# Performance work log

Measured on AMD Instinct MI355X. Metric: run time of the kernel, lower is better.

Reference implementation:

```python
import jax, jax.numpy as jnp
import numpy as np

N_NODES = 100000
N_EDGES = 1600000
D_IN = 128
D_OUT = 128


def setup_inputs() -> dict:
    key = jax.random.key(0)
    k1, k2, k3, k4, k5 = jax.random.split(key, 5)
    features = jax.random.normal(k1, (N_NODES, D_IN), dtype=jnp.float32)
    edge_row = jax.random.randint(k2, (N_EDGES,), 0, N_NODES, dtype=jnp.int32)
    edge_col = jax.random.randint(k3, (N_EDGES,), 0, N_NODES, dtype=jnp.int32)
    edge_val = jax.random.uniform(k4, (N_EDGES,), dtype=jnp.float32)
    # Xavier-uniform weight, zero bias, ones skip weight (matches reset_parameters)
    limit = float(np.sqrt(6.0 / (D_IN + D_OUT)))
    weight = jax.random.uniform(k5, (D_IN, D_OUT), minval=-limit, maxval=limit, dtype=jnp.float32)
    bias = jnp.zeros((D_OUT,), dtype=jnp.float32)
    skip_weight = jnp.ones((D_OUT,), dtype=jnp.float32)
    return {"features": features, "edge_row": edge_row, "edge_col": edge_col,
            "edge_val": edge_val, "weight": weight, "bias": bias,
            "skip_weight": skip_weight}


def reference(features, edge_row, edge_col, edge_val, weight, bias, skip_weight):
    # Dense projection: [N, Din] @ [Din, Dout] -> [N, Dout]
    h = features @ weight
    # SpMM in COO form: Ah[r] = sum_e val[e] * h[col[e]] for edges with row[e]==r
    gathered = edge_val[:, None] * h[edge_col]          # [E, Dout]
    Ah = jax.ops.segment_sum(gathered, edge_row, num_segments=N_NODES)
    # Skip-scale + bias + activation epilogue
    out = h * skip_weight[None, :] + Ah + bias[None, :]
    return jax.nn.selu(out)
```

## Files before the change

### kernel.cpp

```cpp
#include <hip/hip_runtime.h>

#define N_NODES 100000
#define N_EDGES 1600000
#define D 128
#define BM 64
#define GEMM_BLKS 1563

#define BROWS 128
#define NB 782
#define EB 250
#define EPB 6400
#define NTAB (NB * EB)
#define SCAN_BLKS 191

#define SPMM_BLKS 6250

typedef __attribute__((ext_vector_type(8))) short short8_t;
typedef __attribute__((ext_vector_type(4))) float float4_t;
typedef __attribute__((ext_vector_type(2))) float f32x2_t;

__device__ __forceinline__ unsigned pack_bf16x2(float a, float b) {
    unsigned ua = __float_as_uint(a);
    unsigned ub = __float_as_uint(b);
    ua = (ua + 0x7fffu + ((ua >> 16) & 1u)) >> 16;
    ub = (ub + 0x7fffu + ((ub >> 16) & 1u)) & 0xffff0000u;
    return ua | ub;
}

__device__ __forceinline__ float selu_f(float x) {
    const float SCALE = 1.0507009873554805f;
    const float ALPHA = 1.6732632423543772f;
    return x > 0.f ? SCALE * x : SCALE * ALPHA * (expf(x) - 1.f);
}

__global__ __launch_bounds__(256) void bhist_prep_kernel(
    const int* __restrict__ erow, const float* __restrict__ W,
    unsigned* __restrict__ tbl, unsigned short* __restrict__ wt)
{
    __shared__ unsigned hcnt[NB];
    const int t = threadIdx.x;
    if (blockIdx.x < EB) {
        const int k = blockIdx.x;
        for (int i = t; i < NB; i += 256) hcnt[i] = 0;
        __syncthreads();
        const int4* q = (const int4*)(erow + k * EPB);
        for (int i = t; i < EPB / 4; i += 256) {
            const int4 r = q[i];
            atomicAdd(&hcnt[r.x >> 7], 1u);
            atomicAdd(&hcnt[r.y >> 7], 1u);
            atomicAdd(&hcnt[r.z >> 7], 1u);
            atomicAdd(&hcnt[r.w >> 7], 1u);
        }
        __syncthreads();
        for (int i = t; i < NB; i += 256) tbl[k * NB + i] = hcnt[i];
    } else {
        const int pb = blockIdx.x - EB;
        for (int idx = pb * 4096 + t; idx < (pb + 1) * 4096; idx += 256) {
            const int k = idx >> 7, n = idx & 127;
            unsigned u = __float_as_uint(W[idx]);
            u = (u + 0x7fffu + ((u >> 16) & 1u)) >> 16;
            wt[n * D + k] = (unsigned short)u;
        }
    }
}

__global__ __launch_bounds__(1024) void scan_local_kernel(
    const unsigned* __restrict__ tbl, unsigned* __restrict__ lex,
    unsigned* __restrict__ bsum)
{
    __shared__ unsigned wsum[16];
    const int t = threadIdx.x;
    const int L = blockIdx.x * 1024 + t;
    const int lane = t & 63;

    unsigned v = 0;
    if (L < NTAB) {
        const int b = L / EB;
        const int k = L - b * EB;
        v = tbl[k * NB + b];
    }
    unsigned x = v;
#pragma unroll
    for (int d = 1; d < 64; d <<= 1) {
        const unsigned y = __shfl_up(x, d, 64);
        if (lane >= d) x += y;
    }
    if (lane == 63) wsum[t >> 6] = x;
    __syncthreads();
    unsigned add = 0;
    for (int w = 0; w < (t >> 6); ++w) add += wsum[w];
    x += add;
    if (L < NTAB) lex[L] = x - v;
    if (t == 1023) bsum[blockIdx.x] = x;
}

__global__ __launch_bounds__(1024) void scan_apply_kernel(
    const unsigned* __restrict__ lex, const unsigned* __restrict__ bsum,
    unsigned* __restrict__ tbl)
{
    __shared__ unsigned ssum[16];
    __shared__ unsigned offs;
    const int t = threadIdx.x;

    unsigned v = (t < SCAN_BLKS && t < (int)blockIdx.x) ? bsum[t] : 0u;
#pragma unroll
    for (int d = 32; d >= 1; d >>= 1) v += __shfl_down(v, d, 64);
    if ((t & 63) == 0) ssum[t >> 6] = v;
    __syncthreads();
    if (t == 0) {
        unsigned s = 0;
#pragma unroll
        for (int i = 0; i < 16; ++i) s += ssum[i];
        offs = s;
    }
    __syncthreads();

    const int L = blockIdx.x * 1024 + t;
    if (L >= NTAB) return;
    const int b = L / EB;
    const int k = L - b * EB;
    tbl[k * NB + b] = lex[L] + offs;
}

__global__ __launch_bounds__(256) void gemm_scatter_kernel(
    const float* __restrict__ feat, const unsigned short* __restrict__ wt,
    unsigned* __restrict__ h16,
    const int* __restrict__ erow, const int* __restrict__ ecol,
    const float* __restrict__ eval_, const unsigned* __restrict__ tbl,
    int2* __restrict__ rec)
{
    __shared__ __align__(16) char smem[52224];
    const int t = threadIdx.x;

    if (blockIdx.x < GEMM_BLKS) {
        short* At = (short*)smem;
        short* Wt = (short*)(smem + 17408);
        const int rowBase = blockIdx.x * BM;

        {
            const int n = t >> 1, hf = t & 1;
            const uint4* src = (const uint4*)(wt + n * D + hf * 64);
            uint4* dst = (uint4*)&Wt[n * 136 + hf * 64];
#pragma unroll
            for (int j = 0; j < 8; ++j) dst[j] = src[j];
        }
        {
#pragma unroll
            for (int i = 0; i < 8; ++i) {
                const int p = t + 256 * i;
                const int r = p >> 5, kq = p & 31;
                int row = rowBase + r;
                if (row >= N_NODES) row = N_NODES - 1;
                const float4 f = *(const float4*)&feat[(size_t)row * D + kq * 4];
                uint2 u;
                u.x = pack_bf16x2(f.x, f.y);
                u.y = pack_bf16x2(f.z, f.w);
                *(uint2*)&At[r * 136 + kq * 4] = u;
            }
        }
        __syncthreads();

        const int w = t >> 6, lane = t & 63;
        const int m16 = lane & 15, kg = lane >> 4;

        short8_t a_frag[4];
        const int arow = w * 16 + m16;
#pragma unroll
        for (int k0 = 0; k0 < 4; ++k0)
            a_frag[k0] = *(const short8_t*)&At[arow * 136 + k0 * 32 + kg * 8];

#pragma unroll
        for (int nt = 0; nt < 8; ++nt) {
            float4_t acc = {0.f, 0.f, 0.f, 0.f};
#pragma unroll
            for (int k0 = 0; k0 < 4; ++k0) {
                const short8_t b =
                    *(const short8_t*)&Wt[(nt * 16 + m16) * 136 + k0 * 32 + kg * 8];
                acc = __builtin_amdgcn_mfma_f32_16x16x32_bf16(a_frag[k0], b, acc, 0, 0, 0);
            }
            float mine[4], part[4];
#pragma unroll
            for (int i = 0; i < 4; ++i) {
                mine[i] = acc[i];
                part[i] = __shfl_xor(mine[i], 1, 64);
            }
            if ((m16 & 1) == 0) {
                const int cp = (nt * 16 + m16) >> 1;
#pragma unroll
                for (int i = 0; i < 4; ++i) {
                    const int row = rowBase + w * 16 + kg * 4 + i;
                    if (row < N_NODES)
                        h16[(size_t)row * 64 + cp] = pack_bf16x2(mine[i], part[i]);
                }
            }
        }
    } else {
        unsigned* rk = (unsigned*)smem;
        const int k = blockIdx.x - GEMM_BLKS;
        for (int i = t; i < NB; i += 256) rk[i] = 0;
        __syncthreads();

        const int4*   qr = (const int4*)(erow + k * EPB);
        const int4*   qc = (const int4*)(ecol + k * EPB);
        const float4* qv = (const float4*)(eval_ + k * EPB);
        const unsigned* base = tbl + k * NB;

        for (int i = t; i < EPB / 4; i += 256) {
            const int4   r = qr[i];
            const int4   c = qc[i];
            const float4 v = qv[i];
            {
                const int b = r.x >> 7;
                const unsigned pos = base[b] + atomicAdd(&rk[b], 1u);
                rec[pos] = make_int2(c.x | ((r.x & 127) << 17), __float_as_int(v.x));
            }
            {
                const int b = r.y >> 7;
                const unsigned pos = base[b] + atomicAdd(&rk[b], 1u);
                rec[pos] = make_int2(c.y | ((r.y & 127) << 17), __float_as_int(v.y));
            }
            {
                const int b = r.z >> 7;
                const unsigned pos = base[b] + atomicAdd(&rk[b], 1u);
                rec[pos] = make_int2(c.z | ((r.z & 127) << 17), __float_as_int(v.z));
            }
            {
                const int b = r.w >> 7;
                const unsigned pos = base[b] + atomicAdd(&rk[b], 1u);
                rec[pos] = make_int2(c.w | ((r.w & 127) << 17), __float_as_int(v.w));
            }
        }
    }
}

__global__ __launch_bounds__(256) void bsort_kernel(
    const unsigned* __restrict__ tbl, const int2* __restrict__ rec,
    int2* __restrict__ rec2, unsigned* __restrict__ rstart)
{
    __shared__ unsigned cnt[BROWS], base[BROWS], rk[BROWS];
    __shared__ unsigned w0tot;
    const int t = threadIdx.x, b = blockIdx.x;
    if (t < BROWS) { cnt[t] = 0; rk[t] = 0; }
    __syncthreads();

    const unsigned s = tbl[b];
    const unsigned e = (b == NB - 1) ? N_EDGES : tbl[b + 1];

    for (unsigned j = s + t; j < e; j += 256)
        atomicAdd(&cnt[(rec[j].x >> 17) & 127], 1u);
    __syncthreads();

    unsigned v = 0, x = 0;
    if (t < BROWS) {
        v = cnt[t]; x = v;
#pragma unroll
        for (int d = 1; d < 64; d <<= 1) {
            const unsigned y = __shfl_up(x, d, 64);
            if ((t & 63) >= d) x += y;
        }
    }
    if (t == 63) w0tot = x;
    __syncthreads();
    if (t < BROWS) {
        const unsigned ex = x - v + ((t >= 64) ? w0tot : 0u);
        base[t] = s + ex;
        const int row = b * BROWS + t;
        if (row < N_NODES) rstart[row] = s + ex;
    }
    __syncthreads();

    for (unsigned j = s + t; j < e; j += 256) {
        const int2 R = rec[j];
        const int rl = (R.x >> 17) & 127;
        const unsigned pos = base[rl] + atomicAdd(&rk[rl], 1u);
        rec2[pos] = R;
    }
}

__global__ __launch_bounds__(256) void spmm_csr_kernel(
    const unsigned* __restrict__ rstart, const int2* __restrict__ rec,
    const unsigned* __restrict__ h16, const float* __restrict__ skip,
    const float* __restrict__ bias, float* __restrict__ out)
{
    const int lane = threadIdx.x & 63;
    const int wid  = threadIdx.x >> 6;
    const int rowBase = (blockIdx.x * 4 + wid) * 4;

    const int c2 = lane * 2;
    const float2 sk = *(const float2*)&skip[c2];
    const float2 bs = *(const float2*)&bias[c2];

    unsigned sb[5];
#pragma unroll
    for (int i = 0; i < 5; ++i) {
        const int rr = rowBase + i;
        const unsigned bnd = (rr < N_NODES) ? rstart[rr] : (unsigned)N_EDGES;
        sb[i] = (unsigned)__builtin_amdgcn_readfirstlane((int)bnd);
    }

#pragma unroll
    for (int r = 0; r < 4; ++r) {
        const int row = rowBase + r;
        const unsigned s = sb[r];
        const unsigned e = sb[r + 1];
        const unsigned n = e - s;
        const unsigned nfull = n >> 3;

        float ax = 0.f, ay = 0.f, bx = 0.f, by = 0.f;

        int2 E0[8], E1[8];
        unsigned g0[8], g1[8];

        auto LOADREC = [&](int2 (&E)[8], unsigned base) {
#pragma unroll
            for (int k = 0; k < 8; ++k) E[k] = rec[base + k];
        };
        auto GATHER = [&](unsigned (&g)[8], const int2 (&E)[8]) {
#pragma unroll
            for (int k = 0; k < 8; ++k)
                g[k] = h16[(size_t)(((unsigned)E[k].x) & 0x1FFFFu) * 64 + lane];
        };
        auto FMA8 = [&](const int2 (&E)[8], const unsigned (&g)[8]) {
#pragma unroll
            for (int k = 0; k < 8; ++k) {
                const float v = __int_as_float(E[k].y);
                if (k & 1) {
                    bx = fmaf(v, __uint_as_float(g[k] << 16), bx);
                    by = fmaf(v, __uint_as_float(g[k] & 0xffff0000u), by);
                } else {
                    ax = fmaf(v, __uint_as_float(g[k] << 16), ax);
                    ay = fmaf(v, __uint_as_float(g[k] & 0xffff0000u), ay);
                }
            }
        };

        if (nfull) {
            LOADREC(E0, s);
            GATHER(g0, E0);
            unsigned bi = 1;
            for (; bi + 1 < nfull; bi += 2) {
                LOADREC(E1, s + bi * 8);
                GATHER(g1, E1);
                FMA8(E0, g0);
                LOADREC(E0, s + (bi + 1) * 8);
                GATHER(g0, E0);
                FMA8(E1, g1);
            }
            if (bi < nfull) {
                LOADREC(E1, s + bi * 8);
                GATHER(g1, E1);
                FMA8(E0, g0);
                FMA8(E1, g1);
            } else {
                FMA8(E0, g0);
            }
        }

        const unsigned tn = n & 7;
        if (tn) {
            const unsigned tb = s + nfull * 8;
            int2 Et[8];
            unsigned gt[8];
#pragma unroll
            for (int k = 0; k < 8; ++k) {
                const unsigned idx = tb + (unsigned)k;
                Et[k] = rec[idx < e ? idx : e - 1u];
            }
#pragma unroll
            for (int k = 0; k < 8; ++k)
                gt[k] = h16[(size_t)(((unsigned)Et[k].x) & 0x1FFFFu) * 64 + lane];
#pragma unroll
            for (int k = 0; k < 8; ++k) {
                const float v = (tb + (unsigned)k < e) ? __int_as_float(Et[k].y) : 0.f;
                if (k & 1) {
                    bx = fmaf(v, __uint_as_float(gt[k] << 16), bx);
                    by = fmaf(v, __uint_as_float(gt[k] & 0xffff0000u), by);
                } else {
                    ax = fmaf(v, __uint_as_float(gt[k] << 16), ax);
                    ay = fmaf(v, __uint_as_float(gt[k] & 0xffff0000u), ay);
                }
            }
        }

        const unsigned hw = h16[(size_t)row * 64 + lane];
        float ox = fmaf(__uint_as_float(hw << 16),         sk.x, (ax + bx) + bs.x);
        float oy = fmaf(__uint_as_float(hw & 0xffff0000u), sk.y, (ay + by) + bs.y);
        ox = selu_f(ox);
        oy = selu_f(oy);
        f32x2_t o;
        o.x = ox;
        o.y = oy;
        __builtin_nontemporal_store(o, (f32x2_t*)&out[(size_t)row * D + c2]);
    }
}

__global__ __launch_bounds__(256) void gemm_fb_kernel(
    const float* __restrict__ feat, const float* __restrict__ W,
    const float* __restrict__ bias, const float* __restrict__ skip,
    float* __restrict__ h, float* __restrict__ out)
{
    __shared__ float Wl[D * D];
    __shared__ float Fl[32 * D];
    const int tid = threadIdx.x;

    const float4* W4 = (const float4*)W;
    float4* Wl4 = (float4*)Wl;
#pragma unroll
    for (int i = 0; i < 16; ++i) Wl4[tid + 256 * i] = W4[tid + 256 * i];

    const size_t rowBase = (size_t)blockIdx.x * 32;
    const float4* F4 = (const float4*)(feat + rowBase * D);
    float4* Fl4 = (float4*)Fl;
#pragma unroll
    for (int i = 0; i < 4; ++i) Fl4[tid + 256 * i] = F4[tid + 256 * i];
    __syncthreads();

    const int colg = (tid & 31) * 4;
    const int row0 = (tid >> 5) * 4;
    float4 acc[4];
#pragma unroll
    for (int r = 0; r < 4; ++r) acc[r] = make_float4(0.f, 0.f, 0.f, 0.f);
#pragma unroll 4
    for (int k = 0; k < D; ++k) {
        const float4 w = *(const float4*)&Wl[k * D + colg];
#pragma unroll
        for (int r = 0; r < 4; ++r) {
            const float aa = Fl[(row0 + r) * D + k];
            acc[r].x += aa * w.x; acc[r].y += aa * w.y;
            acc[r].z += aa * w.z; acc[r].w += aa * w.w;
        }
    }
    const float4 sk = *(const float4*)&skip[colg];
    const float4 bs = *(const float4*)&bias[colg];
#pragma unroll
    for (int r = 0; r < 4; ++r) {
        const size_t row = rowBase + row0 + r;
        *(float4*)&h[row * D + colg] = acc[r];
        float4 o;
        o.x = acc[r].x * sk.x + bs.x; o.y = acc[r].y * sk.y + bs.y;
        o.z = acc[r].z * sk.z + bs.z; o.w = acc[r].w * sk.w + bs.w;
        *(float4*)&out[row * D + colg] = o;
    }
}

__global__ __launch_bounds__(256) void spmm_atomic_kernel(
    const int* __restrict__ erow, const int* __restrict__ ecol,
    const float* __restrict__ eval_, const float* __restrict__ h,
    float* __restrict__ out)
{
    const int e = blockIdx.x * 4 + (threadIdx.x >> 6);
    if (e >= N_EDGES) return;
    const int lane = threadIdx.x & 63;
    const int r = erow[e];
    const int c = ecol[e];
    const float v = eval_[e];
    const float2 hv = *(const float2*)&h[(size_t)c * D + lane * 2];
    float* o = &out[(size_t)r * D + lane * 2];
    atomicAdd(o + 0, v * hv.x);
    atomicAdd(o + 1, v * hv.y);
}

__global__ __launch_bounds__(256) void selu_kernel(float* __restrict__ out)
{
    const size_t i = (size_t)blockIdx.x * blockDim.x + threadIdx.x;
    float4 v = ((float4*)out)[i];
    v.x = selu_f(v.x); v.y = selu_f(v.y); v.z = selu_f(v.z); v.w = selu_f(v.w);
    ((float4*)out)[i] = v;
}

extern "C" void kernel_launch(void* const* d_in, const int* in_sizes, int n_in,
                              void* d_out, int out_size, void* d_ws, size_t ws_size,
                              hipStream_t stream)
{
    const float* feat  = (const float*)d_in[0];
    const int*   erow  = (const int*)d_in[1];
    const int*   ecol  = (const int*)d_in[2];
    const float* eval_ = (const float*)d_in[3];
    const float* W     = (const float*)d_in[4];
    const float* bias  = (const float*)d_in[5];
    const float* skip  = (const float*)d_in[6];

    float* out = (float*)d_out;

    const size_t off_h16  = 0;
    const size_t off_tbl  = 25600000;
    const size_t off_lex  = 26382000;
    const size_t off_bs   = 27164336;
    const size_t off_rst  = 27165360;
    const size_t off_wt   = 27565360;
    const size_t off_rec  = 27598128;
    const size_t off_rec2 = 40398128;
    const size_t needed   = 53198128;

    char* ws = (char*)d_ws;
    unsigned*       h16    = (unsigned*)(ws + off_h16);
    unsigned*       tbl    = (unsigned*)(ws + off_tbl);
    unsigned*       lex    = (unsigned*)(ws + off_lex);
    unsigned*       bsum   = (unsigned*)(ws + off_bs);
    unsigned*       rstart = (unsigned*)(ws + off_rst);
    unsigned short* wt     = (unsigned short*)(ws + off_wt);
    int2*           rec    = (int2*)(ws + off_rec);
    int2*           rec2   = (int2*)(ws + off_rec2);

    if (ws_size >= needed) {
        bhist_prep_kernel<<<EB + 4, 256, 0, stream>>>(erow, W, tbl, wt);
        scan_local_kernel<<<SCAN_BLKS, 1024, 0, stream>>>(tbl, lex, bsum);
        scan_apply_kernel<<<SCAN_BLKS, 1024, 0, stream>>>(lex, bsum, tbl);
        gemm_scatter_kernel<<<GEMM_BLKS + EB, 256, 0, stream>>>(
            feat, wt, h16, erow, ecol, eval_, tbl, rec);
        bsort_kernel<<<NB, 256, 0, stream>>>(tbl, rec, rec2, rstart);
        spmm_csr_kernel<<<SPMM_BLKS, 256, 0, stream>>>(
            rstart, rec2, h16, skip, bias, out);
    } else {
        float* h = (float*)d_ws;
        gemm_fb_kernel<<<N_NODES / 32, 256, 0, stream>>>(feat, W, bias, skip, h, out);
        spmm_atomic_kernel<<<N_EDGES / 4, 256, 0, stream>>>(erow, ecol, eval_, h, out);
        selu_kernel<<<(N_NODES * D) / (256 * 4), 256, 0, stream>>>(out);
    }
}
```

Baseline: 134.7 us.

## Interleave SpMM gathers across four rows per wavefront to raise memory parallelism

Replaces the per-row software-pipelined gather loop with a joint loop that processes up to eight edges from each of the four rows a wave owns in every iteration. All record loads and gathers for the four rows are issued before the FMAs, so up to 32 gathers are in flight at once instead of 8–16 from a single row. Each chunk is masked with a tail predicate, which drops the separate full and tail paths. In exchange it uses more registers (4x8 records and gathers live at once), which may lower occupancy, and it loses the double-buffered prefetch across iterations.

```diff
diff --git a/kernel.cpp b/kernel.cpp
--- a/kernel.cpp
+++ b/kernel.cpp
@@ -298,93 +298,70 @@
         sb[i] = (unsigned)__builtin_amdgcn_readfirstlane((int)bnd);
     }
 
+    unsigned cur[4], end_[4];
+    float ax[4], ay[4], bx[4], by[4];
+#pragma unroll
+    for (int r = 0; r < 4; ++r) {
+        cur[r] = sb[r];
+        end_[r] = sb[r + 1];
+        ax[r] = 0.f; ay[r] = 0.f; bx[r] = 0.f; by[r] = 0.f;
+    }
+
+    bool more = (cur[0] < end_[0]) | (cur[1] < end_[1]) |
+                (cur[2] < end_[2]) | (cur[3] < end_[3]);
+    while (more) {
+        int2 Ebuf[4][8];
+        unsigned gbuf[4][8];
+        bool act[4];
+
+#pragma unroll
+        for (int r = 0; r < 4; ++r) {
+            act[r] = cur[r] < end_[r];
+            if (act[r]) {
+#pragma unroll
+                for (int k = 0; k < 8; ++k) {
+                    const unsigned idx = cur[r] + (unsigned)k;
+                    Ebuf[r][k] = rec[idx < end_[r] ? idx : end_[r] - 1u];
+                }
+            }
+        }
+#pragma unroll
+        for (int r = 0; r < 4; ++r) {
+            if (act[r]) {
+#pragma unroll
+                for (int k = 0; k < 8; ++k)
+                    gbuf[r][k] =
+                        h16[(size_t)(((unsigned)Ebuf[r][k].x) & 0x1FFFFu) * 64 + lane];
+            }
+        }
+        more = false;
+#pragma unroll
+        for (int r = 0; r < 4; ++r) {
+            if (act[r]) {
+#pragma unroll
+                for (int k = 0; k < 8; ++k) {
+                    const float v = (cur[r] + (unsigned)k < end_[r])
+                                        ? __int_as_float(Ebuf[r][k].y) : 0.f;
+                    if (k & 1) {
+                        bx[r] = fmaf(v, __uint_as_float(gbuf[r][k] << 16), bx[r]);
+                        by[r] = fmaf(v, __uint_as_float(gbuf[r][k] & 0xffff0000u), by[r]);
+                    } else {
+                        ax[r] = fmaf(v, __uint_as_float(gbuf[r][k] << 16), ax[r]);
+                        ay[r] = fmaf(v, __uint_as_float(gbuf[r][k] & 0xffff0000u), ay[r]);
+                    }
+                }
+                cur[r] += 8;
+            }
+            more = more || (cur[r] < end_[r]);
+        }
+    }
+
 #pragma unroll
     for (int r = 0; r < 4; ++r) {
         const int row = rowBase + r;
-        const unsigned s = sb[r];
-        const unsigned e = sb[r + 1];
-        const unsigned n = e - s;
-        const unsigned nfull = n >> 3;
-
-        float ax = 0.f, ay = 0.f, bx = 0.f, by = 0.f;
-
-        int2 E0[8], E1[8];
-        unsigned g0[8], g1[8];
-
-        auto LOADREC = [&](int2 (&E)[8], unsigned base) {
-#pragma unroll
-            for (int k = 0; k < 8; ++k) E[k] = rec[base + k];
-        };
-        auto GATHER = [&](unsigned (&g)[8], const int2 (&E)[8]) {
-#pragma unroll
-            for (int k = 0; k < 8; ++k)
-                g[k] = h16[(size_t)(((unsigned)E[k].x) & 0x1FFFFu) * 64 + lane];
-        };
-        auto FMA8 = [&](const int2 (&E)[8], const unsigned (&g)[8]) {
-#pragma unroll
-            for (int k = 0; k < 8; ++k) {
-                const float v = __int_as_float(E[k].y);
-                if (k & 1) {
-                    bx = fmaf(v, __uint_as_float(g[k] << 16), bx);
-                    by = fmaf(v, __uint_as_float(g[k] & 0xffff0000u), by);
-                } else {
-                    ax = fmaf(v, __uint_as_float(g[k] << 16), ax);
-                    ay = fmaf(v, __uint_as_float(g[k] & 0xffff0000u), ay);
-                }
-            }
-        };
-
-        if (nfull) {
-            LOADREC(E0, s);
-            GATHER(g0, E0);
-            unsigned bi = 1;
-            for (; bi + 1 < nfull; bi += 2) {
-                LOADREC(E1, s + bi * 8);
-                GATHER(g1, E1);
-                FMA8(E0, g0);
-                LOADREC(E0, s + (bi + 1) * 8);
-                GATHER(g0, E0);
-                FMA8(E1, g1);
-            }
-            if (bi < nfull) {
-                LOADREC(E1, s + bi * 8);
-                GATHER(g1, E1);
-                FMA8(E0, g0);
-                FMA8(E1, g1);
-            } else {
-                FMA8(E0, g0);
-            }
-        }
-
-        const unsigned tn = n & 7;
-        if (tn) {
-            const unsigned tb = s + nfull * 8;
-            int2 Et[8];
-            unsigned gt[8];
-#pragma unroll
-            for (int k = 0; k < 8; ++k) {
-                const unsigned idx = tb + (unsigned)k;
-                Et[k] = rec[idx < e ? idx : e - 1u];
-            }
-#pragma unroll
-            for (int k = 0; k < 8; ++k)
-                gt[k] = h16[(size_t)(((unsigned)Et[k].x) & 0x1FFFFu) * 64 + lane];
-#pragma unroll
-            for (int k = 0; k < 8; ++k) {
-                const float v = (tb + (unsigned)k < e) ? __int_as_float(Et[k].y) : 0.f;
-                if (k & 1) {
-                    bx = fmaf(v, __uint_as_float(gt[k] << 16), bx);
-                    by = fmaf(v, __uint_as_float(gt[k] & 0xffff0000u), by);
-                } else {
-                    ax = fmaf(v, __uint_as_float(gt[k] << 16), ax);
-                    ay = fmaf(v, __uint_as_float(gt[k] & 0xffff0000u), ay);
-                }
-            }
-        }
-
         const unsigned hw = h16[(size_t)row * 64 + lane];
-        float ox = fmaf(__uint_as_float(hw << 16),         sk.x, (ax + bx) + bs.x);
-        float oy = fmaf(__uint_as_float(hw & 0xffff0000u), sk.y, (ay + by) + bs.y);
+        float ox = fmaf(__uint_as_float(hw << 16),         sk.x, (ax[r] + bx[r]) + bs.x);
+        float oy = fmaf(__uint_as_float(hw & 0xffff0000u), sk.y, (ay[r] + by[r]) + bs.y);
         ox = selu_f(ox);
         oy = selu_f(oy);
         f32x2_t o;
```

Result: slower. 141.5 us (+5.0%).

## Fuse scan-apply into bucket scatter and overlap GEMM with bucket sort

Applied to the files above, without the earlier changes.

The scan-apply step is folded into a new bucket-scatter kernel. Each scatter block rebuilds the block prefix from bsum and reads its bucket bases straight from lex, keeping them in shared memory instead of a global table. The GEMM is then paired with the per-bucket sort in one launch instead of with the scatter, so the sort's irregular memory work overlaps the compute-bound projection. This removes one kernel launch and one table round trip. In exchange, the scatter now runs alone with only 250 blocks, which may underfill the GPU.

```diff
diff --git a/kernel.cpp b/kernel.cpp
--- a/kernel.cpp
+++ b/kernel.cpp
@@ -94,40 +94,83 @@
     if (t == 1023) bsum[blockIdx.x] = x;
 }
 
-__global__ __launch_bounds__(1024) void scan_apply_kernel(
-    const unsigned* __restrict__ lex, const unsigned* __restrict__ bsum,
-    unsigned* __restrict__ tbl)
-{
-    __shared__ unsigned ssum[16];
-    __shared__ unsigned offs;
+__global__ __launch_bounds__(256) void bscatter_kernel(
+    const int* __restrict__ erow, const int* __restrict__ ecol,
+    const float* __restrict__ eval_, const unsigned* __restrict__ lex,
+    const unsigned* __restrict__ bsum, unsigned* __restrict__ tbl,
+    int2* __restrict__ rec)
+{
+    __shared__ unsigned bp[192];
+    __shared__ unsigned wtot[4];
+    __shared__ unsigned base[NB], rk[NB];
     const int t = threadIdx.x;
-
-    unsigned v = (t < SCAN_BLKS && t < (int)blockIdx.x) ? bsum[t] : 0u;
-#pragma unroll
-    for (int d = 32; d >= 1; d >>= 1) v += __shfl_down(v, d, 64);
-    if ((t & 63) == 0) ssum[t >> 6] = v;
+    const int k = blockIdx.x;
+
+    unsigned v = 0, x = 0;
+    if (t < 192) {
+        v = (t < SCAN_BLKS) ? bsum[t] : 0u;
+        x = v;
+#pragma unroll
+        for (int d = 1; d < 64; d <<= 1) {
+            const unsigned y = __shfl_up(x, d, 64);
+            if ((t & 63) >= d) x += y;
+        }
+        if ((t & 63) == 63) wtot[t >> 6] = x;
+    }
     __syncthreads();
-    if (t == 0) {
-        unsigned s = 0;
-#pragma unroll
-        for (int i = 0; i < 16; ++i) s += ssum[i];
-        offs = s;
+    if (t < 192) {
+        unsigned add = 0;
+        if (t >= 64)  add += wtot[0];
+        if (t >= 128) add += wtot[1];
+        bp[t] = x - v + add;
     }
     __syncthreads();
 
-    const int L = blockIdx.x * 1024 + t;
-    if (L >= NTAB) return;
-    const int b = L / EB;
-    const int k = L - b * EB;
-    tbl[k * NB + b] = lex[L] + offs;
-}
-
-__global__ __launch_bounds__(256) void gemm_scatter_kernel(
+    for (int b = t; b < NB; b += 256) {
+        const int L = b * EB + k;
+        const unsigned bs_ = lex[L] + bp[L >> 10];
+        base[b] = bs_;
+        rk[b] = 0;
+        if (k == 0) tbl[b] = bs_;
+    }
+    __syncthreads();
+
+    const int4*   qr = (const int4*)(erow + k * EPB);
+    const int4*   qc = (const int4*)(ecol + k * EPB);
+    const float4* qv = (const float4*)(eval_ + k * EPB);
+
+    for (int i = t; i < EPB / 4; i += 256) {
+        const int4   r = qr[i];
+        const int4   c = qc[i];
+        const float4 vv = qv[i];
+        {
+            const int b = r.x >> 7;
+            const unsigned pos = base[b] + atomicAdd(&rk[b], 1u);
+            rec[pos] = make_int2(c.x | ((r.x & 127) << 17), __float_as_int(vv.x));
+        }
+        {
+            const int b = r.y >> 7;
+            const unsigned pos = base[b] + atomicAdd(&rk[b], 1u);
+            rec[pos] = make_int2(c.y | ((r.y & 127) << 17), __float_as_int(vv.y));
+        }
+        {
+            const int b = r.z >> 7;
+            const unsigned pos = base[b] + atomicAdd(&rk[b], 1u);
+            rec[pos] = make_int2(c.z | ((r.z & 127) << 17), __float_as_int(vv.z));
+        }
+        {
+            const int b = r.w >> 7;
+            const unsigned pos = base[b] + atomicAdd(&rk[b], 1u);
+            rec[pos] = make_int2(c.w | ((r.w & 127) << 17), __float_as_int(vv.w));
+        }
+    }
+}
+
+__global__ __launch_bounds__(256) void gemm_bsort_kernel(
     const float* __restrict__ feat, const unsigned short* __restrict__ wt,
     unsigned* __restrict__ h16,
-    const int* __restrict__ erow, const int* __restrict__ ecol,
-    const float* __restrict__ eval_, const unsigned* __restrict__ tbl,
-    int2* __restrict__ rec)
+    const unsigned* __restrict__ tbl, const int2* __restrict__ rec,
+    int2* __restrict__ rec2, unsigned* __restrict__ rstart)
 {
     __shared__ __align__(16) char smem[52224];
     const int t = threadIdx.x;
@@ -195,85 +238,47 @@
             }
         }
     } else {
-        unsigned* rk = (unsigned*)smem;
-        const int k = blockIdx.x - GEMM_BLKS;
-        for (int i = t; i < NB; i += 256) rk[i] = 0;
-        __syncthreads();
-
-        const int4*   qr = (const int4*)(erow + k * EPB);
-        const int4*   qc = (const int4*)(ecol + k * EPB);
-        const float4* qv = (const float4*)(eval_ + k * EPB);
-        const unsigned* base = tbl + k * NB;
-
-        for (int i = t; i < EPB / 4; i += 256) {
-            const int4   r = qr[i];
-            const int4   c = qc[i];
-            const float4 v = qv[i];
-            {
-                const int b = r.x >> 7;
-                const unsigned pos = base[b] + atomicAdd(&rk[b], 1u);
-                rec[pos] = make_int2(c.x | ((r.x & 127) << 17), __float_as_int(v.x));
-            }
-            {
-                const int b = r.y >> 7;
-                const unsigned pos = base[b] + atomicAdd(&rk[b], 1u);
-                rec[pos] = make_int2(c.y | ((r.y & 127) << 17), __float_as_int(v.y));
-            }
-            {
-                const int b = r.z >> 7;
-                const unsigned pos = base[b] + atomicAdd(&rk[b], 1u);
-                rec[pos] = make_int2(c.z | ((r.z & 127) << 17), __float_as_int(v.z));
-            }
-            {
-                const int b = r.w >> 7;
-                const unsigned pos = base[b] + atomicAdd(&rk[b], 1u);
-                rec[pos] = make_int2(c.w | ((r.w & 127) << 17), __float_as_int(v.w));
-            }
-        }
-    }
-}
-
-__global__ __launch_bounds__(256) void bsort_kernel(
-    const unsigned* __restrict__ tbl, const int2* __restrict__ rec,
-    int2* __restrict__ rec2, unsigned* __restrict__ rstart)
-{
-    __shared__ unsigned cnt[BROWS], base[BROWS], rk[BROWS];
-    __shared__ unsigned w0tot;
-    const int t = threadIdx.x, b = blockIdx.x;
-    if (t < BROWS) { cnt[t] = 0; rk[t] = 0; }
-    __syncthreads();
-
-    const unsigned s = tbl[b];
-    const unsigned e = (b == NB - 1) ? N_EDGES : tbl[b + 1];
-
-    for (unsigned j = s + t; j < e; j += 256)
-        atomicAdd(&cnt[(rec[j].x >> 17) & 127], 1u);
-    __syncthreads();
-
-    unsigned v = 0, x = 0;
-    if (t < BROWS) {
-        v = cnt[t]; x = v;
-#pragma unroll
-        for (int d = 1; d < 64; d <<= 1) {
-            const unsigned y = __shfl_up(x, d, 64);
-            if ((t & 63) >= d) x += y;
-        }
-    }
-    if (t == 63) w0tot = x;
-    __syncthreads();
-    if (t < BROWS) {
-        const unsigned ex = x - v + ((t >= 64) ? w0tot : 0u);
-        base[t] = s + ex;
-        const int row = b * BROWS + t;
-        if (row < N_NODES) rstart[row] = s + ex;
-    }
-    __syncthreads();
-
-    for (unsigned j = s + t; j < e; j += 256) {
-        const int2 R = rec[j];
-        const int rl = (R.x >> 17) & 127;
-        const unsigned pos = base[rl] + atomicAdd(&rk[rl], 1u);
-        rec2[pos] = R;
+        unsigned* cnt  = (unsigned*)smem;
+        unsigned* bas  = cnt + BROWS;
+        unsigned* rk   = bas + BROWS;
+        unsigned* w0p  = rk + BROWS;
+        const int b = blockIdx.x - GEMM_BLKS;
+
+        if (t < BROWS) { cnt[t] = 0; rk[t] = 0; }
+        __syncthreads();
+
+        const unsigned s = tbl[b];
+        const unsigned e = (b == NB - 1) ? (unsigned)N_EDGES : tbl[b + 1];
+
+        for (unsigned j = s + t; j < e; j += 256)
+            atomicAdd(&cnt[(rec[j].x >> 17) & 127], 1u);
+        __syncthreads();
+
+        unsigned v = 0, x = 0;
+        if (t < BROWS) {
+            v = cnt[t]; x = v;
+#pragma unroll
+            for (int d = 1; d < 64; d <<= 1) {
+                const unsigned y = __shfl_up(x, d, 64);
+                if ((t & 63) >= d) x += y;
+            }
+        }
+        if (t == 63) w0p[0] = x;
+        __syncthreads();
+        if (t < BROWS) {
+            const unsigned ex = x - v + ((t >= 64) ? w0p[0] : 0u);
+            bas[t] = s + ex;
+            const int row = b * BROWS + t;
+            if (row < N_NODES) rstart[row] = s + ex;
+        }
+        __syncthreads();
+
+        for (unsigned j = s + t; j < e; j += 256) {
+            const int2 R = rec[j];
+            const int rl = (R.x >> 17) & 127;
+            const unsigned pos = bas[rl] + atomicAdd(&rk[rl], 1u);
+            rec2[pos] = R;
+        }
     }
 }
 
@@ -505,10 +510,9 @@
     if (ws_size >= needed) {
         bhist_prep_kernel<<<EB + 4, 256, 0, stream>>>(erow, W, tbl, wt);
         scan_local_kernel<<<SCAN_BLKS, 1024, 0, stream>>>(tbl, lex, bsum);
-        scan_apply_kernel<<<SCAN_BLKS, 1024, 0, stream>>>(lex, bsum, tbl);
-        gemm_scatter_kernel<<<GEMM_BLKS + EB, 256, 0, stream>>>(
-            feat, wt, h16, erow, ecol, eval_, tbl, rec);
-        bsort_kernel<<<NB, 256, 0, stream>>>(tbl, rec, rec2, rstart);
+        bscatter_kernel<<<EB, 256, 0, stream>>>(erow, ecol, eval_, lex, bsum, tbl, rec);
+        gemm_bsort_kernel<<<GEMM_BLKS + NB, 256, 0, stream>>>(
+            feat, wt, h16, tbl, rec, rec2, rstart);
         spmm_csr_kernel<<<SPMM_BLKS, 256, 0, stream>>>(
             rstart, rec2, h16, skip, bias, out);
     } else {
```

Measured after the change: 125.5 us, median of 2. 6.8% less time.
